# Kernel optimization log

Measured on AMD Instinct MI355X. Metric: run time of the kernel, lower is better.

Reference implementation:

```python
import jax, jax.numpy as jnp
import numpy as np

HEADS = 16
KEY_SIZE = 64
SIZE_PER_HEAD = 64
OUT_DIM = HEADS * SIZE_PER_HEAD  # 1024
BIG = 1e10
B, LQ, LK = 2, 2048, 2048


def setup_inputs() -> dict:
    key = jax.random.key(0)
    ks = jax.random.split(key, 8)
    q = jax.random.normal(ks[0], (B, LQ, OUT_DIM), dtype=jnp.float32)
    k = jax.random.normal(ks[1], (B, LK, OUT_DIM), dtype=jnp.float32)
    v = jax.random.normal(ks[2], (B, LK, OUT_DIM), dtype=jnp.float32)
    v_mask = (jax.random.uniform(ks[3], (B, LK)) > 0.1).astype(jnp.float32)
    q_mask = (jax.random.uniform(ks[4], (B, LQ)) > 0.1).astype(jnp.float32)
    # bias-free Linear weights, torch layout [out_features, in_features]
    s = 1.0 / np.sqrt(OUT_DIM)
    Wq = jax.random.normal(ks[5], (HEADS * KEY_SIZE, OUT_DIM), dtype=jnp.float32) * s
    Wk = jax.random.normal(ks[6], (HEADS * KEY_SIZE, OUT_DIM), dtype=jnp.float32) * s
    Wv = jax.random.normal(ks[7], (OUT_DIM, OUT_DIM), dtype=jnp.float32) * s
    return {"q": q, "k": k, "v": v, "v_mask": v_mask, "q_mask": q_mask,
            "Wq": Wq, "Wk": Wk, "Wv": Wv}


def _attention(q, k, v, v_mask, q_mask, Wq, Wk, Wv):
    b, lq, _ = q.shape
    lk = k.shape[1]
    # projections (torch Linear: x @ W.T)
    qw = jnp.einsum('bld,ed->ble', q, Wq).reshape(b, lq, HEADS, KEY_SIZE)
    kw = jnp.einsum('bld,ed->ble', k, Wk).reshape(b, lk, HEADS, KEY_SIZE)
    vw = jnp.einsum('bld,ed->ble', v, Wv).reshape(b, lk, HEADS, SIZE_PER_HEAD)
    # scores [B, H, Lq, Lk]
    a = jnp.einsum('bqhd,bkhd->bhqk', qw, kw) / np.sqrt(KEY_SIZE).astype(np.float32)
    # additive key-padding mask: a - (1 - v_mask) * BIG, broadcast over H and Lq
    a = a - (1.0 - v_mask)[:, None, None, :] * BIG
    # mask_right=True branch: mask = (1 - triu(ones, diag=1)) * BIG, i.e. lower
    # triangle INCLUDING the diagonal is penalized (faithful to source quirk).
    causal = jnp.tril(jnp.ones((lq, lk), dtype=a.dtype)) * BIG  # [Lq, Lk]
    a = a - causal[None, None, :, :]
    a = jax.nn.softmax(a, axis=-1)
    # output [B, Lq, H*dv]
    o = jnp.einsum('bhqk,bkhd->bqhd', a, vw).reshape(b, lq, OUT_DIM)
    o = o * q_mask[:, :, None]
    return o


def reference(q, k, v, v_mask, q_mask, Wq, Wk, Wv):
    return _attention(q, k, v, v_mask, q_mask, Wq, Wk, Wv)
```

## Files before the change

### kernel.cpp

```cpp
#include <hip/hip_runtime.h>
#include <hip/hip_bf16.h>
#include <stdint.h>

#define B_   2
#define SEQ  2048
#define EMB  1024
#define BIGF 1e10f

typedef unsigned short u16;
typedef __attribute__((ext_vector_type(4))) u16      u16x4;
typedef __attribute__((ext_vector_type(8))) short    bf8;
typedef __attribute__((ext_vector_type(4))) float    f4;
typedef __attribute__((ext_vector_type(4))) float    fv4;

__device__ inline float bf2f(u16 u){ union{uint32_t i; float f;} v; v.i = ((uint32_t)u) << 16; return v.f; }
__device__ inline u16 f2bf(float f){ union{float f; uint32_t i;} v; v.f = f;
                                     uint32_t r = v.i + 0x7fffu + ((v.i >> 16) & 1u); return (u16)(r >> 16); }

__device__ inline void gl_lds16(const void* g, void* l){
  __builtin_amdgcn_global_load_lds((const __attribute__((address_space(1))) uint32_t*)g,
                                   (__attribute__((address_space(3))) uint32_t*)l, 16, 0, 0);
}

struct CvtArgs { const float* src[6]; u16* dst[6]; int n[6]; };

__global__ __launch_bounds__(256) void cvt_bf16(CvtArgs a)
{
  const int seg = blockIdx.y;
  const float* __restrict__ s = a.src[seg];
  u16* __restrict__ d = a.dst[seg];
  const int n = a.n[seg];
  const int i = (blockIdx.x * 256 + threadIdx.x) * 8;
  if (i >= n) return;
  fv4 x0 = *(const fv4*)(s + i);
  fv4 x1 = *(const fv4*)(s + i + 4);
  union { bf8 v; u16 u[8]; } o;
#pragma unroll
  for (int j = 0; j < 4; j++) { o.u[j] = f2bf(x0[j]); o.u[4 + j] = f2bf(x1[j]); }
  *(bf8*)(d + i) = o.v;
}

__global__ __launch_bounds__(256) void proj_gemm(
    const u16* __restrict__ Xq, const u16* __restrict__ Xk, const u16* __restrict__ Xv,
    const u16* __restrict__ Wq, const u16* __restrict__ Wk, const u16* __restrict__ Wv,
    u16* __restrict__ QH, u16* __restrict__ KH, u16* __restrict__ VTB)
{
  __shared__ u16 smem[18432];
  u16* lA = smem;
  u16* lB = smem + 4096;

  const int z = blockIdx.z;
  const u16* X = (z == 0) ? Xq : ((z == 1) ? Xk : Xv);
  const u16* W = (z == 0) ? Wq : ((z == 1) ? Wk : Wv);

  const int tid  = threadIdx.x;
  const int lane = tid & 63;
  const int w    = tid >> 6;
  const int wm   = w >> 1, wn = w & 1;
  const int m0   = blockIdx.x * 128;
  const int n0   = blockIdx.y * 128;

  const f4 zero = {0.f, 0.f, 0.f, 0.f};
  f4 acc[4][4];
#pragma unroll
  for (int i = 0; i < 4; i++)
#pragma unroll
    for (int j = 0; j < 4; j++) acc[i][j] = zero;

  for (int k0 = 0; k0 < 1024; k0 += 32) {
    __syncthreads();
#pragma unroll
    for (int j = 0; j < 2; j++) {
      const int c = j * 256 + tid;
      const int row = c >> 2, cc = (c & 3) * 8;
      gl_lds16(X + (size_t)(m0 + row) * 1024 + k0 + cc, &lA[(j * 256 + w * 64) * 8]);
      gl_lds16(W + (size_t)(n0 + row) * 1024 + k0 + cc, &lB[(j * 256 + w * 64) * 8]);
    }
    __syncthreads();
    const int koff = (lane >> 4) * 8;
    bf8 a[4], b[4];
#pragma unroll
    for (int t = 0; t < 4; t++) a[t] = *(const bf8*)&lA[(wm * 64 + t * 16 + (lane & 15)) * 32 + koff];
#pragma unroll
    for (int t = 0; t < 4; t++) b[t] = *(const bf8*)&lB[(wn * 64 + t * 16 + (lane & 15)) * 32 + koff];
#pragma unroll
    for (int mt = 0; mt < 4; mt++)
#pragma unroll
      for (int nt = 0; nt < 4; nt++)
        acc[mt][nt] = __builtin_amdgcn_mfma_f32_16x16x32_bf16(a[mt], b[nt], acc[mt][nt], 0, 0, 0);
  }

  __syncthreads();
  const int col = lane & 15, quad = lane >> 4;
  u16* ep = &smem[w * 4608];

  if (z == 2) {
#pragma unroll
    for (int mt = 0; mt < 4; mt++)
#pragma unroll
      for (int nt = 0; nt < 4; nt++) {
        u16x4 pk = { f2bf(acc[mt][nt][0]), f2bf(acc[mt][nt][1]),
                     f2bf(acc[mt][nt][2]), f2bf(acc[mt][nt][3]) };
        *(u16x4*)&ep[(nt * 16 + col) * 72 + mt * 16 + quad * 4] = pk;
      }
  } else {
#pragma unroll
    for (int mt = 0; mt < 4; mt++)
#pragma unroll
      for (int nt = 0; nt < 4; nt++)
#pragma unroll
        for (int r = 0; r < 4; r++)
          ep[(mt * 16 + quad * 4 + r) * 72 + nt * 16 + col] = f2bf(acc[mt][nt][r]);
  }

  const int bb = m0 >> 11;
  const int h  = (n0 >> 6) + wn;
  const int bh = bb * 16 + h;

  if (z == 0) {
    const int qbase = (m0 & 2047) + wm * 64;
    u16* dst = QH + ((size_t)bh * SEQ + qbase) * 64;
#pragma unroll
    for (int i = 0; i < 8; i++) {
      const int f  = i * 1024 + lane * 16;
      const int ml = i * 8 + (lane >> 3), nl = (lane & 7) * 8;
      *(bf8*)(dst + (f >> 1)) = *(const bf8*)&ep[ml * 72 + nl];
    }
  } else if (z == 1) {
    const int kt = (((m0 & 2047) >> 6) + wm);
    u16* dst = KH + (((size_t)bh * 32 + kt) << 12);
#pragma unroll
    for (int i = 0; i < 8; i++) {
      const int f   = i * 1024 + lane * 16;
      const int dh  = f >> 12;
      const int klc = (f >> 6) & 63;
      const int dlo = (lane & 3) * 8;
      *(bf8*)(dst + (f >> 1)) = *(const bf8*)&ep[klc * 72 + dh * 32 + dlo];
    }
  } else {
    const int kt = (((m0 & 2047) >> 6) + wm);
    u16* dst = VTB + (((size_t)bh * 32 + kt) << 12);
#pragma unroll
    for (int i = 0; i < 8; i++) {
      const int f   = i * 1024 + lane * 16;
      const int kk  = f >> 12;
      const int d   = (f >> 6) & 63;
      const int klo = (lane & 3) * 8;
      *(bf8*)(dst + (f >> 1)) = *(const bf8*)&ep[d * 72 + kk * 32 + klo];
    }
  }
}

__global__ __launch_bounds__(256) void sumv(const u16* __restrict__ VTB,
                                            const float* __restrict__ vmask,
                                            float* __restrict__ fb)
{
  const int w = threadIdx.x >> 6, lane = threadIdx.x & 63;
  const int gw = blockIdx.x * 4 + w;
  const int b = gw >> 10, e = gw & 1023;
  const int h = e >> 6, d = e & 63;
  const int bh = b * 16 + h;
  const float* vm = vmask + b * SEQ;
  float s = 0.f, c = 0.f;
  for (int kt = 0; kt < 32; kt++) {
    const u16 val = VTB[(((size_t)bh * 32 + kt) << 12) + (lane >> 5) * 2048 + d * 32 + (lane & 31)];
    const float m = vm[kt * 64 + lane];
    s += m * bf2f(val); c += m;
  }
#pragma unroll
  for (int o = 1; o < 64; o <<= 1) { s += __shfl_xor(s, o); c += __shfl_xor(c, o); }
  if (lane == 0) fb[gw] = s / c;
}

__global__ __launch_bounds__(256) void attn(
    const u16* __restrict__ QH, const u16* __restrict__ KH, const u16* __restrict__ VTB,
    const float* __restrict__ vmask, const float* __restrict__ qmask,
    const float* __restrict__ fb, float* __restrict__ OUT)
{
  __shared__ float pen[SEQ];
  __shared__ u16   sK[4096];
  __shared__ u16   sV[4096];
  __shared__ u16   P[4 * 16 * 72];

  const int tid = threadIdx.x, lane = tid & 63, w = tid >> 6;
  const int b = blockIdx.z, h = blockIdx.y;
  const int qx = (blockIdx.x + blockIdx.y) & 31;
  const int q0 = qx * 64;
  const int bh = b * 16 + h;
  const int col = lane & 15, quad = lane >> 4;
  const int wb = w * 16 * 72;

  for (int i = tid; i < SEQ; i += 256)
    pen[i] = (1.0f - vmask[b * SEQ + i]) * BIGF;

  bf8 aQ[2];
#pragma unroll
  for (int dh = 0; dh < 2; dh++)
    aQ[dh] = *(const bf8*)&QH[((size_t)bh * SEQ + q0 + w * 16 + col) * 64 + dh * 32 + quad * 8];

  const f4 zero = {0.f, 0.f, 0.f, 0.f};
  f4 accO[4];
  float l_part[4] = {0.f, 0.f, 0.f, 0.f};
#pragma unroll
  for (int t = 0; t < 4; t++) accO[t] = zero;

  for (int kt = qx; kt < 32; kt++) {
    __syncthreads();
    {
      const u16* kb = KH  + (((size_t)bh * 32 + kt) << 12);
      const u16* vb = VTB + (((size_t)bh * 32 + kt) << 12);
#pragma unroll
      for (int i = 0; i < 2; i++) {
        const int off = w * 1024 + i * 512;
        gl_lds16(kb + off + lane * 8, &sK[off]);
        gl_lds16(vb + off + lane * 8, &sV[off]);
      }
    }
    __syncthreads();

    f4 accS[4];
#pragma unroll
    for (int t = 0; t < 4; t++) accS[t] = zero;
#pragma unroll
    for (int nt = 0; nt < 4; nt++)
#pragma unroll
      for (int dh = 0; dh < 2; dh++) {
        bf8 bK = *(const bf8*)&sK[dh * 2048 + (nt * 16 + col) * 32 + quad * 8];
        accS[nt] = __builtin_amdgcn_mfma_f32_16x16x32_bf16(aQ[dh], bK, accS[nt], 0, 0, 0);
      }

    const int k0 = kt * 64;
    float pen4[4];
#pragma unroll
    for (int nt = 0; nt < 4; nt++) pen4[nt] = pen[k0 + nt * 16 + col];
    float p[4][4];
    if (kt == qx) {
#pragma unroll
      for (int nt = 0; nt < 4; nt++)
#pragma unroll
        for (int r = 0; r < 4; r++) {
          float sv = accS[nt][r] * 0.125f - pen4[nt];
          if (nt * 16 + col <= w * 16 + quad * 4 + r) sv -= BIGF;
          p[nt][r] = __expf(sv);
        }
    } else {
#pragma unroll
      for (int nt = 0; nt < 4; nt++)
#pragma unroll
        for (int r = 0; r < 4; r++)
          p[nt][r] = __expf(accS[nt][r] * 0.125f - pen4[nt]);
    }
#pragma unroll
    for (int r = 0; r < 4; r++)
      l_part[r] += (p[0][r] + p[1][r]) + (p[2][r] + p[3][r]);

#pragma unroll
    for (int nt = 0; nt < 4; nt++)
#pragma unroll
      for (int rp = 0; rp < 4; rp += 2) {
        float2 f2c; f2c.x = p[nt][rp]; f2c.y = p[nt][rp + 1];
        union { __hip_bfloat162 h2; u16 u[2]; } cv;
        cv.h2 = __float22bfloat162_rn(f2c);
        P[wb + (quad * 4 + rp    ) * 72 + nt * 16 + col] = cv.u[0];
        P[wb + (quad * 4 + rp + 1) * 72 + nt * 16 + col] = cv.u[1];
      }

#pragma unroll
    for (int kk = 0; kk < 2; kk++) {
      bf8 aP = *(const bf8*)&P[wb + col * 72 + kk * 32 + quad * 8];
#pragma unroll
      for (int nt = 0; nt < 4; nt++) {
        bf8 bV = *(const bf8*)&sV[kk * 2048 + (nt * 16 + col) * 32 + quad * 8];
        accO[nt] = __builtin_amdgcn_mfma_f32_16x16x32_bf16(aP, bV, accO[nt], 0, 0, 0);
      }
    }
  }

#pragma unroll
  for (int r = 0; r < 4; r++) {
    float l = l_part[r];
    l += __shfl_xor(l, 1); l += __shfl_xor(l, 2);
    l += __shfl_xor(l, 4); l += __shfl_xor(l, 8);
    const int q = q0 + w * 16 + quad * 4 + r;
    const float qm = qmask[b * SEQ + q];
    float* op = OUT + (size_t)(b * SEQ + q) * EMB + h * 64;
    if (l == 0.0f) {
#pragma unroll
      for (int nt = 0; nt < 4; nt++)
        op[nt * 16 + col] = fb[b * 1024 + h * 64 + nt * 16 + col] * qm;
    } else {
      const float s = qm / l;
#pragma unroll
      for (int nt = 0; nt < 4; nt++)
        op[nt * 16 + col] = accO[nt][r] * s;
    }
  }
}

extern "C" void kernel_launch(void* const* d_in, const int* in_sizes, int n_in,
                              void* d_out, int out_size, void* d_ws, size_t ws_size,
                              hipStream_t stream)
{
  const float* q  = (const float*)d_in[0];
  const float* k  = (const float*)d_in[1];
  const float* v  = (const float*)d_in[2];
  const float* vm = (const float*)d_in[3];
  const float* qm = (const float*)d_in[4];
  const float* Wq = (const float*)d_in[5];
  const float* Wk = (const float*)d_in[6];
  const float* Wv = (const float*)d_in[7];
  float* out = (float*)d_out;

  const size_t NBIG = (size_t)B_ * SEQ * EMB;
  const size_t NW   = (size_t)EMB * EMB;

  u16* qb  = (u16*)d_ws;
  u16* kb  = qb  + NBIG;
  u16* vb  = kb  + NBIG;
  u16* Wqb = vb  + NBIG;
  u16* Wkb = Wqb + NW;
  u16* Wvb = Wkb + NW;
  u16* QH  = Wvb + NW;
  u16* KH  = QH  + NBIG;
  u16* VTB = KH  + NBIG;
  float* fb = (float*)(VTB + NBIG);

  CvtArgs ca;
  ca.src[0] = q;  ca.dst[0] = qb;  ca.n[0] = (int)NBIG;
  ca.src[1] = k;  ca.dst[1] = kb;  ca.n[1] = (int)NBIG;
  ca.src[2] = v;  ca.dst[2] = vb;  ca.n[2] = (int)NBIG;
  ca.src[3] = Wq; ca.dst[3] = Wqb; ca.n[3] = (int)NW;
  ca.src[4] = Wk; ca.dst[4] = Wkb; ca.n[4] = (int)NW;
  ca.src[5] = Wv; ca.dst[5] = Wvb; ca.n[5] = (int)NW;

  cvt_bf16<<<dim3((unsigned)(NBIG / 8 / 256), 6, 1), 256, 0, stream>>>(ca);
  proj_gemm<<<dim3(32, 8, 3), 256, 0, stream>>>(qb, kb, vb, Wqb, Wkb, Wvb, QH, KH, VTB);
  sumv<<<dim3(512, 1, 1), 256, 0, stream>>>(VTB, vm, fb);
  attn<<<dim3(32, 16, 2), 256, 0, stream>>>(QH, KH, VTB, vm, qm, fb, out);
}
```

Baseline: 221.3 us.

## Pair causal q-tiles per block, double-buffer K/V, XCD-aware mapping, exp2

Each block now handles two complementary query tiles (qpair and 31-qpair), so the causal work per block is equal. Blocks are remapped so that all tiles of one batch-head land on the same XCD, which improves L2 reuse of K/V. K/V tiles are double-buffered in LDS, with the next tile's async load issued before computing on the current one, and one of the two barriers per iteration is removed. The softmax uses a hardware exp2 with log2e folded into the scale and the penalty, at the cost of doubled LDS for K/V and half as many blocks.

```diff
diff --git a/kernel.cpp b/kernel.cpp
--- a/kernel.cpp
+++ b/kernel.cpp
@@ -2,10 +2,13 @@
 #include <hip/hip_bf16.h>
 #include <stdint.h>
 
-#define B_   2
-#define SEQ  2048
-#define EMB  1024
-#define BIGF 1e10f
+#define B_    2
+#define SEQ   2048
+#define EMB   1024
+#define BIGF  1e10f
+#define LOG2E 1.4426950408889634f
+#define BIG2F (1e10f * LOG2E)
+#define C2    (0.125f * LOG2E)
 
 typedef unsigned short u16;
 typedef __attribute__((ext_vector_type(4))) u16      u16x4;
@@ -16,6 +19,7 @@
 __device__ inline float bf2f(u16 u){ union{uint32_t i; float f;} v; v.i = ((uint32_t)u) << 16; return v.f; }
 __device__ inline u16 f2bf(float f){ union{float f; uint32_t i;} v; v.f = f;
                                      uint32_t r = v.i + 0x7fffu + ((v.i >> 16) & 1u); return (u16)(r >> 16); }
+__device__ inline float exp2_hw(float x){ float r; asm("v_exp_f32 %0, %1" : "=v"(r) : "v"(x)); return r; }
 
 __device__ inline void gl_lds16(const void* g, void* l){
   __builtin_amdgcn_global_load_lds((const __attribute__((address_space(1))) uint32_t*)g,
@@ -178,121 +182,140 @@
     const float* __restrict__ fb, float* __restrict__ OUT)
 {
   __shared__ float pen[SEQ];
-  __shared__ u16   sK[4096];
-  __shared__ u16   sV[4096];
+  __shared__ u16   sK[2][4096];
+  __shared__ u16   sV[2][4096];
   __shared__ u16   P[4 * 16 * 72];
 
   const int tid = threadIdx.x, lane = tid & 63, w = tid >> 6;
-  const int b = blockIdx.z, h = blockIdx.y;
-  const int qx = (blockIdx.x + blockIdx.y) & 31;
-  const int q0 = qx * 64;
-  const int bh = b * 16 + h;
+  const int i   = blockIdx.x;
+  const int xcd = i & 7;
+  const int j   = i >> 3;
+  const int bh  = xcd + 8 * (j >> 4);
+  const int qpair = j & 15;
+  const int b = bh >> 4, h = bh & 15;
   const int col = lane & 15, quad = lane >> 4;
   const int wb = w * 16 * 72;
 
-  for (int i = tid; i < SEQ; i += 256)
-    pen[i] = (1.0f - vmask[b * SEQ + i]) * BIGF;
-
-  bf8 aQ[2];
-#pragma unroll
-  for (int dh = 0; dh < 2; dh++)
-    aQ[dh] = *(const bf8*)&QH[((size_t)bh * SEQ + q0 + w * 16 + col) * 64 + dh * 32 + quad * 8];
-
-  const f4 zero = {0.f, 0.f, 0.f, 0.f};
-  f4 accO[4];
-  float l_part[4] = {0.f, 0.f, 0.f, 0.f};
-#pragma unroll
-  for (int t = 0; t < 4; t++) accO[t] = zero;
-
-  for (int kt = qx; kt < 32; kt++) {
+  for (int t = tid; t < SEQ; t += 256)
+    pen[t] = (1.0f - vmask[b * SEQ + t]) * BIG2F;
+
+  const u16* kbase = KH  + (((size_t)bh * 32) << 12);
+  const u16* vbase = VTB + (((size_t)bh * 32) << 12);
+
+  for (int pass = 0; pass < 2; pass++) {
+    const int qx = pass ? (31 - qpair) : qpair;
+    const int q0 = qx * 64;
+
+    bf8 aQ[2];
+#pragma unroll
+    for (int dh = 0; dh < 2; dh++)
+      aQ[dh] = *(const bf8*)&QH[((size_t)bh * SEQ + q0 + w * 16 + col) * 64 + dh * 32 + quad * 8];
+
+    const f4 zero = {0.f, 0.f, 0.f, 0.f};
+    f4 accO[4];
+    float l_part[4] = {0.f, 0.f, 0.f, 0.f};
+#pragma unroll
+    for (int t = 0; t < 4; t++) accO[t] = zero;
+
     __syncthreads();
     {
-      const u16* kb = KH  + (((size_t)bh * 32 + kt) << 12);
-      const u16* vb = VTB + (((size_t)bh * 32 + kt) << 12);
-#pragma unroll
-      for (int i = 0; i < 2; i++) {
-        const int off = w * 1024 + i * 512;
-        gl_lds16(kb + off + lane * 8, &sK[off]);
-        gl_lds16(vb + off + lane * 8, &sV[off]);
-      }
-    }
-    __syncthreads();
-
-    f4 accS[4];
-#pragma unroll
-    for (int t = 0; t < 4; t++) accS[t] = zero;
-#pragma unroll
-    for (int nt = 0; nt < 4; nt++)
-#pragma unroll
-      for (int dh = 0; dh < 2; dh++) {
-        bf8 bK = *(const bf8*)&sK[dh * 2048 + (nt * 16 + col) * 32 + quad * 8];
-        accS[nt] = __builtin_amdgcn_mfma_f32_16x16x32_bf16(aQ[dh], bK, accS[nt], 0, 0, 0);
-      }
-
-    const int k0 = kt * 64;
-    float pen4[4];
-#pragma unroll
-    for (int nt = 0; nt < 4; nt++) pen4[nt] = pen[k0 + nt * 16 + col];
-    float p[4][4];
-    if (kt == qx) {
+      const size_t toff = ((size_t)qx << 12) + w * 1024 + lane * 8;
+      gl_lds16(kbase + toff,       &sK[0][w * 1024]);
+      gl_lds16(kbase + toff + 512, &sK[0][w * 1024 + 512]);
+      gl_lds16(vbase + toff,       &sV[0][w * 1024]);
+      gl_lds16(vbase + toff + 512, &sV[0][w * 1024 + 512]);
+    }
+
+    const int ntile = 32 - qx;
+    for (int it = 0; it < ntile; it++) {
+      __syncthreads();
+      if (it + 1 < ntile) {
+        const int nb = (it + 1) & 1;
+        const size_t toff = ((size_t)(qx + it + 1) << 12) + w * 1024 + lane * 8;
+        gl_lds16(kbase + toff,       &sK[nb][w * 1024]);
+        gl_lds16(kbase + toff + 512, &sK[nb][w * 1024 + 512]);
+        gl_lds16(vbase + toff,       &sV[nb][w * 1024]);
+        gl_lds16(vbase + toff + 512, &sV[nb][w * 1024 + 512]);
+      }
+      const u16* cK = sK[it & 1];
+      const u16* cV = sV[it & 1];
+      const int k0 = (qx + it) * 64;
+
+      f4 accS[4];
+#pragma unroll
+      for (int t = 0; t < 4; t++) accS[t] = zero;
 #pragma unroll
       for (int nt = 0; nt < 4; nt++)
 #pragma unroll
-        for (int r = 0; r < 4; r++) {
-          float sv = accS[nt][r] * 0.125f - pen4[nt];
-          if (nt * 16 + col <= w * 16 + quad * 4 + r) sv -= BIGF;
-          p[nt][r] = __expf(sv);
+        for (int dh = 0; dh < 2; dh++) {
+          bf8 bK = *(const bf8*)&cK[dh * 2048 + (nt * 16 + col) * 32 + quad * 8];
+          accS[nt] = __builtin_amdgcn_mfma_f32_16x16x32_bf16(aQ[dh], bK, accS[nt], 0, 0, 0);
         }
-    } else {
+
+      float pen4[4];
+#pragma unroll
+      for (int nt = 0; nt < 4; nt++) pen4[nt] = pen[k0 + nt * 16 + col];
+      float p[4][4];
+      if (it == 0) {
+#pragma unroll
+        for (int nt = 0; nt < 4; nt++)
+#pragma unroll
+          for (int r = 0; r < 4; r++) {
+            float sv = fmaf(accS[nt][r], C2, -pen4[nt]);
+            if (nt * 16 + col <= w * 16 + quad * 4 + r) sv -= BIG2F;
+            p[nt][r] = exp2_hw(sv);
+          }
+      } else {
+#pragma unroll
+        for (int nt = 0; nt < 4; nt++)
+#pragma unroll
+          for (int r = 0; r < 4; r++)
+            p[nt][r] = exp2_hw(fmaf(accS[nt][r], C2, -pen4[nt]));
+      }
+#pragma unroll
+      for (int r = 0; r < 4; r++)
+        l_part[r] += (p[0][r] + p[1][r]) + (p[2][r] + p[3][r]);
+
 #pragma unroll
       for (int nt = 0; nt < 4; nt++)
 #pragma unroll
-        for (int r = 0; r < 4; r++)
-          p[nt][r] = __expf(accS[nt][r] * 0.125f - pen4[nt]);
-    }
-#pragma unroll
-    for (int r = 0; r < 4; r++)
-      l_part[r] += (p[0][r] + p[1][r]) + (p[2][r] + p[3][r]);
-
-#pragma unroll
-    for (int nt = 0; nt < 4; nt++)
-#pragma unroll
-      for (int rp = 0; rp < 4; rp += 2) {
-        float2 f2c; f2c.x = p[nt][rp]; f2c.y = p[nt][rp + 1];
-        union { __hip_bfloat162 h2; u16 u[2]; } cv;
-        cv.h2 = __float22bfloat162_rn(f2c);
-        P[wb + (quad * 4 + rp    ) * 72 + nt * 16 + col] = cv.u[0];
-        P[wb + (quad * 4 + rp + 1) * 72 + nt * 16 + col] = cv.u[1];
-      }
-
-#pragma unroll
-    for (int kk = 0; kk < 2; kk++) {
-      bf8 aP = *(const bf8*)&P[wb + col * 72 + kk * 32 + quad * 8];
-#pragma unroll
-      for (int nt = 0; nt < 4; nt++) {
-        bf8 bV = *(const bf8*)&sV[kk * 2048 + (nt * 16 + col) * 32 + quad * 8];
-        accO[nt] = __builtin_amdgcn_mfma_f32_16x16x32_bf16(aP, bV, accO[nt], 0, 0, 0);
-      }
-    }
-  }
-
-#pragma unroll
-  for (int r = 0; r < 4; r++) {
-    float l = l_part[r];
-    l += __shfl_xor(l, 1); l += __shfl_xor(l, 2);
-    l += __shfl_xor(l, 4); l += __shfl_xor(l, 8);
-    const int q = q0 + w * 16 + quad * 4 + r;
-    const float qm = qmask[b * SEQ + q];
-    float* op = OUT + (size_t)(b * SEQ + q) * EMB + h * 64;
-    if (l == 0.0f) {
-#pragma unroll
-      for (int nt = 0; nt < 4; nt++)
-        op[nt * 16 + col] = fb[b * 1024 + h * 64 + nt * 16 + col] * qm;
-    } else {
-      const float s = qm / l;
-#pragma unroll
-      for (int nt = 0; nt < 4; nt++)
-        op[nt * 16 + col] = accO[nt][r] * s;
+        for (int rp = 0; rp < 4; rp += 2) {
+          float2 f2c; f2c.x = p[nt][rp]; f2c.y = p[nt][rp + 1];
+          union { __hip_bfloat162 h2; u16 u[2]; } cv;
+          cv.h2 = __float22bfloat162_rn(f2c);
+          P[wb + (quad * 4 + rp    ) * 72 + nt * 16 + col] = cv.u[0];
+          P[wb + (quad * 4 + rp + 1) * 72 + nt * 16 + col] = cv.u[1];
+        }
+
+#pragma unroll
+      for (int kk = 0; kk < 2; kk++) {
+        bf8 aP = *(const bf8*)&P[wb + col * 72 + kk * 32 + quad * 8];
+#pragma unroll
+        for (int nt = 0; nt < 4; nt++) {
+          bf8 bV = *(const bf8*)&cV[kk * 2048 + (nt * 16 + col) * 32 + quad * 8];
+          accO[nt] = __builtin_amdgcn_mfma_f32_16x16x32_bf16(aP, bV, accO[nt], 0, 0, 0);
+        }
+      }
+    }
+
+#pragma unroll
+    for (int r = 0; r < 4; r++) {
+      float l = l_part[r];
+      l += __shfl_xor(l, 1); l += __shfl_xor(l, 2);
+      l += __shfl_xor(l, 4); l += __shfl_xor(l, 8);
+      const int q = q0 + w * 16 + quad * 4 + r;
+      const float qm = qmask[b * SEQ + q];
+      float* op = OUT + (size_t)(b * SEQ + q) * EMB + h * 64;
+      if (l == 0.0f) {
+#pragma unroll
+        for (int nt = 0; nt < 4; nt++)
+          op[nt * 16 + col] = fb[b * 1024 + h * 64 + nt * 16 + col] * qm;
+      } else {
+        const float s = qm / l;
+#pragma unroll
+        for (int nt = 0; nt < 4; nt++)
+          op[nt * 16 + col] = accO[nt][r] * s;
+      }
     }
   }
 }
@@ -336,5 +359,5 @@
   cvt_bf16<<<dim3((unsigned)(NBIG / 8 / 256), 6, 1), 256, 0, stream>>>(ca);
   proj_gemm<<<dim3(32, 8, 3), 256, 0, stream>>>(qb, kb, vb, Wqb, Wkb, Wvb, QH, KH, VTB);
   sumv<<<dim3(512, 1, 1), 256, 0, stream>>>(VTB, vm, fb);
-  attn<<<dim3(32, 16, 2), 256, 0, stream>>>(QH, KH, VTB, vm, qm, fb, out);
-}
+  attn<<<dim3(512, 1, 1), 256, 0, stream>>>(QH, KH, VTB, vm, qm, fb, out);
+}
```

Measured after the change: 204.4 us. 7.7% less time.
